# Performance work log

Hardware: AMD Instinct MI355X
Metric: run time of the kernel (lower is better)

Reference implementation:

```python
import jax, jax.numpy as jnp
import numpy as np

D_MODEL = 512
HEADS = 8
HEAD_DIM = D_MODEL // HEADS
LN_EPS = 1e-5


def _rel_shift(pos_score):
    # pos_score: [B, H, T, P] with P = 2T-1
    B, H, T, P = pos_score.shape
    padded = jnp.pad(pos_score, ((0, 0), (0, 0), (0, 0), (1, 0)))  # [B,H,T,P+1]
    shifted = padded.reshape(B, H, P + 1, T)[:, :, 1:, :].reshape(B, H, T, P)
    return shifted[:, :, :, : P // 2 + 1]  # [B,H,T,T]


def setup_inputs() -> dict:
    key = jax.random.key(0)
    ks = jax.random.split(key, 16)
    B, T = 16, 512
    P = 2 * T - 1
    s = 1.0 / np.sqrt(D_MODEL)
    inp = {
        "x": jax.random.normal(ks[0], (B, T, D_MODEL), jnp.float32),
        "pos_emb": jax.random.normal(ks[1], (B, P, D_MODEL), jnp.float32),
        "ln_g": jnp.ones((D_MODEL,), jnp.float32),
        "ln_b": jnp.zeros((D_MODEL,), jnp.float32),
        "Wq": jax.random.normal(ks[2], (D_MODEL, D_MODEL), jnp.float32) * s,
        "bq": jnp.zeros((D_MODEL,), jnp.float32),
        "Wk": jax.random.normal(ks[3], (D_MODEL, D_MODEL), jnp.float32) * s,
        "bk": jnp.zeros((D_MODEL,), jnp.float32),
        "Wv": jax.random.normal(ks[4], (D_MODEL, D_MODEL), jnp.float32) * s,
        "bv": jnp.zeros((D_MODEL,), jnp.float32),
        "Wp": jax.random.normal(ks[5], (D_MODEL, D_MODEL), jnp.float32) * s,
        "bp": jnp.zeros((D_MODEL,), jnp.float32),
        "content_bias": jax.random.normal(ks[6], (HEADS, HEAD_DIM), jnp.float32) * 0.05,
        "position_bias": jax.random.normal(ks[7], (HEADS, HEAD_DIM), jnp.float32) * 0.05,
        "Wo": jax.random.normal(ks[8], (D_MODEL, D_MODEL), jnp.float32) * s,
        "bo": jnp.zeros((D_MODEL,), jnp.float32),
    }
    return inp


def reference(x, pos_emb, ln_g, ln_b, Wq, bq, Wk, bk, Wv, bv, Wp, bp,
              content_bias, position_bias, Wo, bo):
    B, T, D = x.shape
    H, hd = HEADS, HEAD_DIM

    # LayerNorm over last dim
    mu = jnp.mean(x, axis=-1, keepdims=True)
    var = jnp.var(x, axis=-1, keepdims=True)
    xn = (x - mu) / jnp.sqrt(var + LN_EPS) * ln_g + ln_b

    q = (xn @ Wq.T + bq).reshape(B, T, H, hd)                 # [B,T,H,hd]
    k = (xn @ Wk.T + bk).reshape(B, T, H, hd)                 # [B,T,H,hd]
    v = (xn @ Wv.T + bv).reshape(B, T, H, hd)                 # [B,T,H,hd]
    p = (pos_emb @ Wp.T + bp).reshape(B, -1, H, hd)           # [B,P,H,hd]

    content_score = jnp.einsum('bshd,bthd->bhst', q + content_bias, k)   # [B,H,T,T]
    pos_score = jnp.einsum('bshd,bphd->bhsp', q + position_bias, p)      # [B,H,T,P]
    pos_score = _rel_shift(pos_score)                                    # [B,H,T,T]

    scores = (content_score + pos_score) / jnp.sqrt(jnp.asarray(hd, x.dtype))
    w = jax.nn.softmax(scores, axis=-1)
    ctx = jnp.einsum('bhst,bthd->bshd', w, v).reshape(B, T, D)
    return ctx @ Wo.T + bo
```

## Files before the change

### kernel.cpp

```cpp
#include <hip/hip_runtime.h>
#include <cstdio>
#include <cstdint>


typedef short s16x8 __attribute__((ext_vector_type(8)));
typedef float f32x4 __attribute__((ext_vector_type(4)));
typedef unsigned short u16x4 __attribute__((ext_vector_type(4)));
typedef unsigned short u16x8 __attribute__((ext_vector_type(8)));

#define CSCALE 0.1803368801111204f

#if __has_builtin(__builtin_amdgcn_exp2f)
#define EXP2(x) __builtin_amdgcn_exp2f(x)
#else
#define EXP2(x) exp2f(x)
#endif

__device__ __forceinline__ unsigned short f2bf(float f) {
  unsigned int u = __builtin_bit_cast(unsigned int, f);
  unsigned int r = (u + 0x7FFFu + ((u >> 16) & 1u)) >> 16;
  return (unsigned short)r;
}
__device__ __forceinline__ float bf2f(unsigned short h) {
  unsigned int u = ((unsigned int)h) << 16;
  return __builtin_bit_cast(float, u);
}
__device__ __forceinline__ size_t pk(int row, int col) {
  return (size_t)(row >> 4) * 8192 + (col >> 5) * 512 + ((col >> 3) & 3) * 128 +
         (row & 15) * 8 + (col & 7);
}

__device__ __forceinline__ void gload_lds16(const unsigned short* g,
                                            unsigned short* l) {
  __builtin_amdgcn_global_load_lds(
      (const __attribute__((address_space(1))) unsigned int*)g,
      (__attribute__((address_space(3))) unsigned int*)l, 16, 0, 0);
}

__global__ __launch_bounds__(256) void megaprep(
    const float* __restrict__ x, const float* __restrict__ g,
    const float* __restrict__ bb, unsigned short* __restrict__ xpk,
    const float* __restrict__ pe, unsigned short* __restrict__ pepk,
    const float* __restrict__ Wq, const float* __restrict__ Wk,
    const float* __restrict__ Wp, const float* __restrict__ Wv,
    const float* __restrict__ Wo, const float* __restrict__ bq,
    const float* __restrict__ bk, unsigned short* __restrict__ wqk,
    unsigned short* __restrict__ wpm, unsigned short* __restrict__ wvm,
    unsigned short* __restrict__ wom, float* __restrict__ bqk) {
  const int bid = blockIdx.x, tid = threadIdx.x;
  if (bid < 2048) {
    const int wave = tid >> 6, lane = tid & 63;
    const int row = bid * 4 + wave;
    const int c0 = lane * 8;
    const float* xr = x + (size_t)row * 512 + c0;
    float4 v0 = *(const float4*)xr;
    float4 v1 = *(const float4*)(xr + 4);
    float vv[8] = {v0.x, v0.y, v0.z, v0.w, v1.x, v1.y, v1.z, v1.w};
    float s = 0.f, ss = 0.f;
#pragma unroll
    for (int j = 0; j < 8; ++j) { s += vv[j]; ss += vv[j] * vv[j]; }
#pragma unroll
    for (int d = 1; d < 64; d <<= 1) {
      s += __shfl_xor(s, d, 64);
      ss += __shfl_xor(ss, d, 64);
    }
    const float mu = s * (1.0f / 512.0f);
    const float var = ss * (1.0f / 512.0f) - mu * mu;
    const float rstd = rsqrtf(var + 1e-5f);
    u16x8 o;
#pragma unroll
    for (int j = 0; j < 8; ++j)
      o[j] = f2bf((vv[j] - mu) * rstd * g[c0 + j] + bb[c0 + j]);
    *(u16x8*)(xpk + pk(row, c0)) = o;
  } else if (bid < 6144) {
    int gid = (bid - 2048) * 256 + tid;
    int e = gid * 8;
    int r = e >> 9, c = e & 511;
    int b = r >> 10, u = r & 1023;
    u16x8 o = {0, 0, 0, 0, 0, 0, 0, 0};
    if (u < 1023) {
      const float* src = pe + (size_t)(b * 1023 + u) * 512 + c;
      float4 v0 = *(const float4*)src;
      float4 v1 = *(const float4*)(src + 4);
      o[0] = f2bf(v0.x); o[1] = f2bf(v0.y); o[2] = f2bf(v0.z); o[3] = f2bf(v0.w);
      o[4] = f2bf(v1.x); o[5] = f2bf(v1.y); o[6] = f2bf(v1.z); o[7] = f2bf(v1.w);
    }
    *(u16x8*)(pepk + (size_t)b * 524288 + pk(u, c)) = o;
  } else {
    int gid = (bid - 6144) * 256 + tid;
    int idx = gid * 8;
    int region = idx >> 18, off = idx & 262143;
    const float* src = (region == 0)   ? Wq
                       : (region == 1) ? Wk
                       : (region == 2) ? Wp
                       : (region == 3) ? Wv
                                       : Wo;
    float4 v0 = *(const float4*)(src + off);
    float4 v1 = *(const float4*)(src + off + 4);
    u16x8 o;
    o[0] = f2bf(v0.x); o[1] = f2bf(v0.y); o[2] = f2bf(v0.z); o[3] = f2bf(v0.w);
    o[4] = f2bf(v1.x); o[5] = f2bf(v1.y); o[6] = f2bf(v1.z); o[7] = f2bf(v1.w);
    int n = off >> 9, k = off & 511;
    unsigned short* dst;
    int nrow = n;
    if (region == 0) { dst = wqk; }
    else if (region == 1) { dst = wqk; nrow = n + 512; }
    else if (region == 2) { dst = wpm; }
    else if (region == 3) { dst = wvm; }
    else { dst = wom; }
    *(u16x8*)(dst + pk(nrow, k)) = o;
    if (idx < 1024) {
#pragma unroll
      for (int j = 0; j < 8; j++) {
        int ii = idx + j;
        bqk[ii] = (ii < 512) ? bq[ii] : bk[ii - 512];
      }
    }
  }
}

template <bool SWAP>
__device__ __forceinline__ void gemm128_p3(
    const unsigned short* __restrict__ Apk, int astrip8,
    const unsigned short* __restrict__ Bpk, int bstrip8,
    unsigned short* __restrict__ lA, unsigned short* __restrict__ lB,
    int wave, int lane, f32x4 acc[4][4]) {
  const int wr = wave >> 1, wc = wave & 1;
  const unsigned short* ga =
      Apk + (size_t)(astrip8 + 2 * wave) * 8192 + lane * 8;
  const unsigned short* gb =
      Bpk + (size_t)(bstrip8 + 2 * wave) * 8192 + lane * 8;
#define STG3(kc, buf)                                                        \
  _Pragma("unroll") for (int s = 0; s < 2; ++s) {                            \
    gload_lds16(ga + (size_t)s * 8192 + (kc) * 512,                          \
                lA + (buf) * 4096 + (2 * wave + s) * 512);                   \
    gload_lds16(gb + (size_t)s * 8192 + (kc) * 512,                          \
                lB + (buf) * 4096 + (2 * wave + s) * 512);                   \
  }
  STG3(0, 0);
  STG3(1, 1);
  const unsigned short* lar = lA + (wr * 4) * 512 + lane * 8;
  const unsigned short* lbr = lB + (wc * 4) * 512 + lane * 8;
#pragma unroll
  for (int kc = 0; kc < 16; ++kc) {
    const int cur = kc % 3;
    if (kc < 14) { STG3(kc + 2, (kc + 2) % 3); }
    if (kc < 14) {
      asm volatile("s_waitcnt vmcnt(8)" ::: "memory");
    } else if (kc == 14) {
      asm volatile("s_waitcnt vmcnt(4)" ::: "memory");
    } else {
      asm volatile("s_waitcnt vmcnt(0)" ::: "memory");
    }
    __builtin_amdgcn_s_barrier();
    __builtin_amdgcn_sched_barrier(0);
    s16x8 af[4], bf[4];
#pragma unroll
    for (int mt = 0; mt < 4; ++mt)
      af[mt] = *(const s16x8*)(lar + cur * 4096 + mt * 512);
#pragma unroll
    for (int nt = 0; nt < 4; ++nt)
      bf[nt] = *(const s16x8*)(lbr + cur * 4096 + nt * 512);
#pragma unroll
    for (int mt = 0; mt < 4; ++mt)
#pragma unroll
      for (int nt = 0; nt < 4; ++nt)
        acc[mt][nt] =
            SWAP ? __builtin_amdgcn_mfma_f32_16x16x32_bf16(
                       bf[nt], af[mt], acc[mt][nt], 0, 0, 0)
                 : __builtin_amdgcn_mfma_f32_16x16x32_bf16(
                       af[mt], bf[nt], acc[mt][nt], 0, 0, 0);
    __builtin_amdgcn_sched_barrier(0);
    __builtin_amdgcn_s_barrier();
  }
#undef STG3
}

__global__ __launch_bounds__(256) void proj_all(
    const unsigned short* __restrict__ xpk, const unsigned short* __restrict__ pepk,
    const unsigned short* __restrict__ wqk, const unsigned short* __restrict__ wpm,
    const unsigned short* __restrict__ wvm, const float* __restrict__ bqk,
    const float* __restrict__ bp, const float* __restrict__ bv,
    const float* __restrict__ cbv, const float* __restrict__ pbv,
    unsigned short* __restrict__ qc, unsigned short* __restrict__ qp,
    unsigned short* __restrict__ kb, unsigned short* __restrict__ pbuf,
    unsigned short* __restrict__ vth) {
  __shared__ __align__(16) unsigned short lA[12288];
  __shared__ __align__(16) unsigned short lB[12288];
  const int tid = threadIdx.x, lane = tid & 63, wave = tid >> 6;
  int bid = blockIdx.x;
  bid = (bid & 7) * 160 + (bid >> 3);
  const int wr = wave >> 1, wc = wave & 1;
  const int fr = lane & 15, hi2 = lane >> 4;
  f32x4 fz = {0.f, 0.f, 0.f, 0.f};
  f32x4 acc[4][4];
#pragma unroll
  for (int i = 0; i < 4; i++)
#pragma unroll
    for (int j = 0; j < 4; j++) acc[i][j] = fz;

  if (bid < 512) {
    int m_t = bid >> 3, n_t = bid & 7;
    gemm128_p3<true>(xpk, m_t * 8, wqk, n_t * 8, lA, lB, wave, lane, acc);
    int m0 = m_t * 128 + wr * 64, n0 = n_t * 128 + wc * 64;
#pragma unroll
    for (int nt = 0; nt < 4; ++nt) {
      int colb = n0 + nt * 16 + hi2 * 4;
      float4 b4 = *(const float4*)(bqk + colb);
      float bvv[4] = {b4.x, b4.y, b4.z, b4.w};
      if (colb < 512) {
        int h = colb >> 6, cc = colb & 63;
        float4 c4 = *(const float4*)(cbv + colb);
        float4 p4 = *(const float4*)(pbv + colb);
        float cvv[4] = {c4.x, c4.y, c4.z, c4.w};
        float pvv[4] = {p4.x, p4.y, p4.z, p4.w};
        size_t cpart = (size_t)(cc >> 5) * 512 + ((cc & 31) >> 3) * 128 +
                       (cc & 7) + (size_t)h * 32768;
#pragma unroll
        for (int mt = 0; mt < 4; ++mt) {
          int row = m0 + mt * 16 + fr;
          int b = row >> 9, s16i = (row & 511) >> 4;
          size_t idx = ((size_t)b * 8 * 32 + s16i) * 1024 + cpart + fr * 8;
          u16x4 oc, op;
#pragma unroll
          for (int r = 0; r < 4; ++r) {
            float val = acc[mt][nt][r] + bvv[r];
            oc[r] = f2bf((val + cvv[r]) * CSCALE);
            op[r] = f2bf((val + pvv[r]) * CSCALE);
          }
          *(u16x4*)(qc + idx) = oc;
          *(u16x4*)(qp + idx) = op;
        }
      } else {
        int c2 = colb - 512, h = c2 >> 6, cc = c2 & 63;
        size_t cpart = (size_t)(cc >> 5) * 512 + ((cc & 31) >> 3) * 128 +
                       (cc & 7) + (size_t)h * 32768;
#pragma unroll
        for (int mt = 0; mt < 4; ++mt) {
          int row = m0 + mt * 16 + fr;
          int b = row >> 9, s16i = (row & 511) >> 4;
          size_t idx = ((size_t)b * 8 * 32 + s16i) * 1024 + cpart + fr * 8;
          u16x4 ok;
#pragma unroll
          for (int r = 0; r < 4; ++r) ok[r] = f2bf(acc[mt][nt][r] + bvv[r]);
          *(u16x4*)(kb + idx) = ok;
        }
      }
    }
  } else if (bid < 1024) {
    int pid = bid - 512;
    int b = pid >> 5, rem = pid & 31;
    int m_tb = rem >> 2, n_t = rem & 3;
    gemm128_p3<true>(pepk + (size_t)b * 524288, m_tb * 8, wpm, n_t * 8, lA,
                     lB, wave, lane, acc);
    int u0 = m_tb * 128 + wr * 64, n0 = n_t * 128 + wc * 64;
#pragma unroll
    for (int nt = 0; nt < 4; ++nt) {
      int colb = n0 + nt * 16 + hi2 * 4;
      float4 b4 = *(const float4*)(bp + colb);
      float bvv[4] = {b4.x, b4.y, b4.z, b4.w};
      int h = colb >> 6, cc = colb & 63;
      size_t cbase = (size_t)(b * 8 + h) * 65536 + (cc >> 5) * 512 +
                     ((cc & 31) >> 3) * 128 + (cc & 7);
#pragma unroll
      for (int mt = 0; mt < 4; ++mt) {
        int u = u0 + mt * 16 + fr;
        size_t idx = cbase + (size_t)(u >> 4) * 1024 + (u & 15) * 8;
        u16x4 o;
        if (u >= 1023) {
          o[0] = 0; o[1] = 0; o[2] = 0; o[3] = 0;
        } else {
#pragma unroll
          for (int r = 0; r < 4; ++r) o[r] = f2bf(acc[mt][nt][r] + bvv[r]);
        }
        *(u16x4*)(pbuf + idx) = o;
      }
    }
  } else {
    int vid = bid - 1024;
    int m_t = vid >> 2, n_t = vid & 3;
    gemm128_p3<false>(xpk, m_t * 8, wvm, n_t * 8, lA, lB, wave, lane, acc);
    int m0 = m_t * 128 + wr * 64, n0 = n_t * 128 + wc * 64;
#pragma unroll
    for (int nt = 0; nt < 4; ++nt) {
      int col = n0 + nt * 16 + fr;
      float bval = bv[col];
      int h = col >> 6, d = col & 63;
#pragma unroll
      for (int mt = 0; mt < 4; ++mt) {
        int rowb = m0 + mt * 16 + hi2 * 4;
        int b = rowb >> 9, t = rowb & 511;
        size_t idx =
            ((size_t)((b * 8 + h) * 4 + (d >> 4)) * 16 + (t >> 5)) * 512 +
            ((t & 31) >> 3) * 128 + (d & 15) * 8 + (t & 7);
        u16x4 hv;
#pragma unroll
        for (int r = 0; r < 4; ++r) hv[r] = f2bf(acc[mt][nt][r] + bval);
        *(u16x4*)(vth + idx) = hv;
      }
    }
  }
}

__global__ __launch_bounds__(256) void out_gemm(
    const unsigned short* __restrict__ ctxpk, const unsigned short* __restrict__ wom,
    const float* __restrict__ bo, float* __restrict__ out) {
  __shared__ __align__(16) unsigned short lA[12288];
  __shared__ __align__(16) unsigned short lB[12288];
  const int tid = threadIdx.x, lane = tid & 63, wave = tid >> 6;
  const int bid = blockIdx.x;
  const int wr = wave >> 1, wc = wave & 1;
  const int fr = lane & 15, hi2 = lane >> 4;
  int m_t = bid >> 2, n_t = bid & 3;
  f32x4 fz = {0.f, 0.f, 0.f, 0.f};
  f32x4 acc[4][4];
#pragma unroll
  for (int i = 0; i < 4; i++)
#pragma unroll
    for (int j = 0; j < 4; j++) acc[i][j] = fz;
  gemm128_p3<true>(ctxpk, m_t * 8, wom, n_t * 8, lA, lB, wave, lane, acc);
  int m0 = m_t * 128 + wr * 64, n0 = n_t * 128 + wc * 64;
#pragma unroll
  for (int nt = 0; nt < 4; ++nt) {
    int colb = n0 + nt * 16 + hi2 * 4;
    float4 b4 = *(const float4*)(bo + colb);
#pragma unroll
    for (int mt = 0; mt < 4; ++mt) {
      int row = m0 + mt * 16 + fr;
      float4 o;
      o.x = acc[mt][nt][0] + b4.x;
      o.y = acc[mt][nt][1] + b4.y;
      o.z = acc[mt][nt][2] + b4.z;
      o.w = acc[mt][nt][3] + b4.w;
      *(float4*)(out + (size_t)row * 512 + colb) = o;
    }
  }
}

__global__ __launch_bounds__(256) void flash_attn(
    const unsigned short* __restrict__ qc, const unsigned short* __restrict__ qp,
    const unsigned short* __restrict__ kb, const unsigned short* __restrict__ pm,
    const unsigned short* __restrict__ vth, unsigned short* __restrict__ ctxpk) {
  const int id = blockIdx.x;
  const int bh = id & 127, b = bh >> 3, h = bh & 7;
  const int s_blk = id >> 7;
  const int tid = threadIdx.x, wave = tid >> 6, lane = tid & 63;
  const int fr = lane & 15, hi2 = lane >> 4, fc = hi2 * 8;
  const int s0w = s_blk * 64 + wave * 16;
  const int crow = hi2 * 4;
  const int pbase0 = 31 - 4 * s_blk;

  __shared__ __align__(16) unsigned short lK[4096];
  __shared__ __align__(16) unsigned short lV[4096];
  __shared__ __align__(16) unsigned short lP[8192];
  __shared__ __align__(16) unsigned short Ph_s[4][16][40];
  unsigned short(*Phw)[40] = Ph_s[wave];

  int srcl[4];
#pragma unroll
  for (int r = 0; r < 4; ++r) srcl[r] = (hi2 << 4) | ((fr - (crow + r) - 1) & 15);

  const size_t qtb = ((size_t)(b * 8 + h) * 32 + (s0w >> 4)) * 1024 + lane * 8;
  s16x8 aqc0 = *(const s16x8*)(qc + qtb);
  s16x8 aqc1 = *(const s16x8*)(qc + qtb + 512);
  s16x8 aqp0 = *(const s16x8*)(qp + qtb);
  s16x8 aqp1 = *(const s16x8*)(qp + qtb + 512);

  const unsigned short* kpk = kb + (size_t)(b * 8 + h) * 32768 + lane * 8;
  const unsigned short* ppk = pm + (size_t)(b * 8 + h) * 65536 + lane * 8;
  const unsigned short* vhk = vth + (size_t)(b * 8 + h) * 32768 + lane * 8;

  if (wave == 0) {
#pragma unroll
    for (int c = 0; c < 4; ++c) gload_lds16(kpk + c * 512, lK + c * 512);
  } else if (wave == 1) {
#pragma unroll
    for (int c = 0; c < 4; ++c)
      gload_lds16(vhk + (size_t)(c * 16) * 512, lV + c * 512);
  } else {
#pragma unroll
    for (int j = 0; j < 3; ++j) {
      const int t = pbase0 - 3 + (wave - 2) * 3 + j;
#pragma unroll
      for (int hf = 0; hf < 2; ++hf)
        gload_lds16(ppk + (size_t)t * 1024 + hf * 512,
                    lP + (t & 7) * 1024 + hf * 512);
    }
  }

  f32x4 fz = {0.f, 0.f, 0.f, 0.f};
  f32x4 Oacc[4] = {fz, fz, fz, fz};
  float lsum[4] = {0.f, 0.f, 0.f, 0.f};

  __syncthreads();

#pragma unroll 2
  for (int s = 0; s < 16; ++s) {
    const int cur = s & 1, nxt = cur ^ 1;
    if (s < 15) {
      const int sn = s + 1;
      if (wave == 0) {
#pragma unroll
        for (int c = 0; c < 4; ++c)
          gload_lds16(kpk + (size_t)(2 * sn) * 1024 + c * 512,
                      lK + nxt * 2048 + c * 512);
      } else if (wave == 1) {
#pragma unroll
        for (int c = 0; c < 4; ++c)
          gload_lds16(vhk + (size_t)(c * 16 + sn) * 512,
                      lV + nxt * 2048 + c * 512);
      } else {
        const int t = pbase0 + 2 * s + 3 + (wave - 2);
#pragma unroll
        for (int hf = 0; hf < 2; ++hf)
          gload_lds16(ppk + (size_t)t * 1024 + hf * 512,
                      lP + (t & 7) * 1024 + hf * 512);
      }
    }
    const unsigned short* lk = lK + cur * 2048 + lane * 8;
    const unsigned short* lv = lV + cur * 2048 + lane * 8;
    s16x8 kf[4], pf[6], vf[4];
#pragma unroll
    for (int nt = 0; nt < 2; ++nt) {
      kf[2 * nt] = *(const s16x8*)(lk + nt * 1024);
      kf[2 * nt + 1] = *(const s16x8*)(lk + nt * 1024 + 512);
    }
#pragma unroll
    for (int nt = 0; nt < 3; ++nt) {
      const int t = pbase0 + 2 * s - wave + nt;
      const unsigned short* lp = lP + (t & 7) * 1024 + lane * 8;
      pf[2 * nt] = *(const s16x8*)lp;
      pf[2 * nt + 1] = *(const s16x8*)(lp + 512);
    }
#pragma unroll
    for (int nt = 0; nt < 4; ++nt) vf[nt] = *(const s16x8*)(lv + nt * 512);

    f32x4 sc[2] = {fz, fz};
    __builtin_amdgcn_s_setprio(1);
#pragma unroll
    for (int nt = 0; nt < 2; ++nt) {
      sc[nt] = __builtin_amdgcn_mfma_f32_16x16x32_bf16(aqc0, kf[2 * nt],
                                                       sc[nt], 0, 0, 0);
      sc[nt] = __builtin_amdgcn_mfma_f32_16x16x32_bf16(aqc1, kf[2 * nt + 1],
                                                       sc[nt], 0, 0, 0);
    }
    f32x4 sp[3];
#pragma unroll
    for (int nt = 0; nt < 3; ++nt) {
      f32x4 t2 = fz;
      t2 = __builtin_amdgcn_mfma_f32_16x16x32_bf16(aqp0, pf[2 * nt], t2, 0, 0, 0);
      t2 = __builtin_amdgcn_mfma_f32_16x16x32_bf16(aqp1, pf[2 * nt + 1], t2, 0, 0, 0);
      sp[nt] = t2;
    }
    __builtin_amdgcn_s_setprio(0);
    float sj[3][4];
#pragma unroll
    for (int j = 0; j < 3; ++j)
#pragma unroll
      for (int r = 0; r < 4; ++r) sj[j][r] = __shfl(sp[j][r], srcl[r], 64);
#pragma unroll
    for (int nt = 0; nt < 2; ++nt) {
      int tc = nt * 16 + fr;
#pragma unroll
      for (int r = 0; r < 4; ++r) {
        float pos = (fr <= crow + r) ? sj[nt][r] : sj[nt + 1][r];
        float e = EXP2(sc[nt][r] + pos);
        lsum[r] += e;
        Phw[crow + r][tc] = f2bf(e);
      }
    }
    s16x8 ah = *(const s16x8*)&Phw[fr][fc];
    __builtin_amdgcn_s_setprio(1);
#pragma unroll
    for (int nt = 0; nt < 4; ++nt)
      Oacc[nt] = __builtin_amdgcn_mfma_f32_16x16x32_bf16(ah, vf[nt], Oacc[nt],
                                                         0, 0, 0);
    __builtin_amdgcn_s_setprio(0);
    __syncthreads();
  }

#pragma unroll
  for (int d = 1; d < 16; d <<= 1)
#pragma unroll
    for (int r = 0; r < 4; ++r) lsum[r] += __shfl_xor(lsum[r], d, 64);
#pragma unroll
  for (int nt = 0; nt < 4; ++nt)
#pragma unroll
    for (int r = 0; r < 4; ++r) {
      float o = Oacc[nt][r] / lsum[r];
      int row = b * 512 + s0w + crow + r;
      int col = h * 64 + nt * 16 + fr;
      ctxpk[pk(row, col)] = f2bf(o);
    }
}

extern "C" void kernel_launch(void* const* d_in, const int* in_sizes, int n_in,
                              void* d_out, int out_size, void* d_ws,
                              size_t ws_size, hipStream_t stream) {
  const float* x = (const float*)d_in[0];
  const float* pe = (const float*)d_in[1];
  const float* ln_g = (const float*)d_in[2];
  const float* ln_b = (const float*)d_in[3];
  const float* Wq = (const float*)d_in[4];
  const float* bq = (const float*)d_in[5];
  const float* Wk = (const float*)d_in[6];
  const float* bk = (const float*)d_in[7];
  const float* Wv = (const float*)d_in[8];
  const float* bv = (const float*)d_in[9];
  const float* Wp = (const float*)d_in[10];
  const float* bp = (const float*)d_in[11];
  const float* cb = (const float*)d_in[12];
  const float* pb = (const float*)d_in[13];
  const float* Wo = (const float*)d_in[14];
  const float* bo = (const float*)d_in[15];
  float* out = (float*)d_out;

  char* ws = (char*)d_ws;
  size_t off = 0;
  auto alloc = [&](size_t bytes) -> char* {
    char* ptr = ws + off;
    off = (off + bytes + 255) & ~(size_t)255;
    return ptr;
  };
  unsigned short* xpk = (unsigned short*)alloc((size_t)8192 * 512 * 2);
  unsigned short* ctxpk = xpk;
  unsigned short* pepk = (unsigned short*)alloc((size_t)16384 * 512 * 2);
  unsigned short* vt_hi = (unsigned short*)alloc((size_t)8192 * 512 * 2);
  unsigned short* wqk = (unsigned short*)alloc((size_t)1024 * 512 * 2);
  unsigned short* wpm = (unsigned short*)alloc((size_t)512 * 512 * 2);
  unsigned short* wvm = (unsigned short*)alloc((size_t)512 * 512 * 2);
  unsigned short* wom = (unsigned short*)alloc((size_t)512 * 512 * 2);
  float* bqk = (float*)alloc(1024 * 4);
  unsigned short* qc = (unsigned short*)alloc((size_t)8192 * 512 * 2);
  unsigned short* qp = (unsigned short*)alloc((size_t)8192 * 512 * 2);
  unsigned short* kbuf = (unsigned short*)alloc((size_t)8192 * 512 * 2);
  unsigned short* pbuf = (unsigned short*)alloc((size_t)16384 * 512 * 2);

  if (ws_size < off) {
    fprintf(stderr, "kernel_launch: ws too small (need %zu, have %zu)\n", off,
            ws_size);
    return;
  }

  megaprep<<<6784, 256, 0, stream>>>(x, ln_g, ln_b, xpk, pe, pepk, Wq, Wk, Wp,
                                     Wv, Wo, bq, bk, wqk, wpm, wvm, wom, bqk);
  proj_all<<<1280, 256, 0, stream>>>(xpk, pepk, wqk, wpm, wvm, bqk, bp, bv,
                                     cb, pb, qc, qp, kbuf, pbuf, vt_hi);
  flash_attn<<<1024, 256, 0, stream>>>(qc, qp, kbuf, pbuf, vt_hi, ctxpk);
  out_gemm<<<256, 256, 0, stream>>>(ctxpk, wom, bo, out);
}
```

Baseline: 207.1 us.

## Triple-buffer K/V/pos tiles in flash attention with explicit vmcnt waits

Moves the flash_attn LDS staging from double to triple buffering: K and V tiles use three slots, and the positional ring grows from 8 to 10 slots. Loads are now issued two iterations ahead. Each __syncthreads is replaced by a partial s_waitcnt vmcnt plus a raw s_barrier, so loads for later tiles can stay in flight while the current one is computed. This raises LDS use per block, which may reduce occupancy. The hand-counted vmcnt values must match the exact number of outstanding loads per wave, so any mismatch would be a correctness risk.

```diff
diff --git a/kernel.cpp b/kernel.cpp
--- a/kernel.cpp
+++ b/kernel.cpp
@@ -350,9 +350,9 @@
   const int crow = hi2 * 4;
   const int pbase0 = 31 - 4 * s_blk;
 
-  __shared__ __align__(16) unsigned short lK[4096];
-  __shared__ __align__(16) unsigned short lV[4096];
-  __shared__ __align__(16) unsigned short lP[8192];
+  __shared__ __align__(16) unsigned short lK[6144];
+  __shared__ __align__(16) unsigned short lV[6144];
+  __shared__ __align__(16) unsigned short lP[10240];
   __shared__ __align__(16) unsigned short Ph_s[4][16][40];
   unsigned short(*Phw)[40] = Ph_s[wave];
 
@@ -373,18 +373,33 @@
   if (wave == 0) {
 #pragma unroll
     for (int c = 0; c < 4; ++c) gload_lds16(kpk + c * 512, lK + c * 512);
+#pragma unroll
+    for (int c = 0; c < 4; ++c)
+      gload_lds16(kpk + (size_t)2 * 1024 + c * 512, lK + 2048 + c * 512);
   } else if (wave == 1) {
 #pragma unroll
     for (int c = 0; c < 4; ++c)
       gload_lds16(vhk + (size_t)(c * 16) * 512, lV + c * 512);
+#pragma unroll
+    for (int c = 0; c < 4; ++c)
+      gload_lds16(vhk + (size_t)(c * 16 + 1) * 512, lV + 2048 + c * 512);
   } else {
 #pragma unroll
     for (int j = 0; j < 3; ++j) {
       const int t = pbase0 - 3 + (wave - 2) * 3 + j;
+      const int sl = t % 10;
 #pragma unroll
       for (int hf = 0; hf < 2; ++hf)
         gload_lds16(ppk + (size_t)t * 1024 + hf * 512,
-                    lP + (t & 7) * 1024 + hf * 512);
+                    lP + sl * 1024 + hf * 512);
+    }
+    {
+      const int t = pbase0 + 3 + (wave - 2);
+      const int sl = t % 10;
+#pragma unroll
+      for (int hf = 0; hf < 2; ++hf)
+        gload_lds16(ppk + (size_t)t * 1024 + hf * 512,
+                    lP + sl * 1024 + hf * 512);
     }
   }
 
@@ -392,31 +407,42 @@
   f32x4 Oacc[4] = {fz, fz, fz, fz};
   float lsum[4] = {0.f, 0.f, 0.f, 0.f};
 
-  __syncthreads();
-
 #pragma unroll 2
   for (int s = 0; s < 16; ++s) {
-    const int cur = s & 1, nxt = cur ^ 1;
-    if (s < 15) {
-      const int sn = s + 1;
+    if (s < 14) {
+      const int sn = s + 2;
+      const int bufn = sn % 3;
       if (wave == 0) {
 #pragma unroll
         for (int c = 0; c < 4; ++c)
           gload_lds16(kpk + (size_t)(2 * sn) * 1024 + c * 512,
-                      lK + nxt * 2048 + c * 512);
+                      lK + bufn * 2048 + c * 512);
       } else if (wave == 1) {
 #pragma unroll
         for (int c = 0; c < 4; ++c)
           gload_lds16(vhk + (size_t)(c * 16 + sn) * 512,
-                      lV + nxt * 2048 + c * 512);
+                      lV + bufn * 2048 + c * 512);
       } else {
-        const int t = pbase0 + 2 * s + 3 + (wave - 2);
+        const int t = pbase0 + 2 * s + 5 + (wave - 2);
+        const int sl = t % 10;
 #pragma unroll
         for (int hf = 0; hf < 2; ++hf)
           gload_lds16(ppk + (size_t)t * 1024 + hf * 512,
-                      lP + (t & 7) * 1024 + hf * 512);
+                      lP + sl * 1024 + hf * 512);
       }
     }
+    if (s < 14) {
+      if (wave < 2) asm volatile("s_waitcnt vmcnt(8)" ::: "memory");
+      else          asm volatile("s_waitcnt vmcnt(4)" ::: "memory");
+    } else if (s == 14) {
+      if (wave < 2) asm volatile("s_waitcnt vmcnt(4)" ::: "memory");
+      else          asm volatile("s_waitcnt vmcnt(2)" ::: "memory");
+    } else {
+      asm volatile("s_waitcnt vmcnt(0)" ::: "memory");
+    }
+    __builtin_amdgcn_s_barrier();
+    __builtin_amdgcn_sched_barrier(0);
+    const int cur = s % 3;
     const unsigned short* lk = lK + cur * 2048 + lane * 8;
     const unsigned short* lv = lV + cur * 2048 + lane * 8;
     s16x8 kf[4], pf[6], vf[4];
@@ -428,7 +454,8 @@
 #pragma unroll
     for (int nt = 0; nt < 3; ++nt) {
       const int t = pbase0 + 2 * s - wave + nt;
-      const unsigned short* lp = lP + (t & 7) * 1024 + lane * 8;
+      const int sl = t % 10;
+      const unsigned short* lp = lP + sl * 1024 + lane * 8;
       pf[2 * nt] = *(const s16x8*)lp;
       pf[2 * nt + 1] = *(const s16x8*)(lp + 512);
     }
@@ -476,7 +503,8 @@
       Oacc[nt] = __builtin_amdgcn_mfma_f32_16x16x32_bf16(ah, vf[nt], Oacc[nt],
                                                          0, 0, 0);
     __builtin_amdgcn_s_setprio(0);
-    __syncthreads();
+    __builtin_amdgcn_sched_barrier(0);
+    __builtin_amdgcn_s_barrier();
   }
 
 #pragma unroll
```

Measured after the change: 210.8 us. About the same (+1.8%).
